# Performance work log

Measured on AMD Instinct MI355X. Metric: run time of the kernel, lower is better.

The kernel has to match this reference:

```python
import jax, jax.numpy as jnp
import numpy as np

B, N = 8, 65536
REG_WEIGHT = 1.0


def box2corners(box):
    # box: (B,N,5) [x,y,w,h,alpha] -> corners (B,N,4,2), CCW order
    x, y, w, h, alpha = (box[..., i] for i in range(5))
    x4 = jnp.asarray([0.5, -0.5, -0.5, 0.5], box.dtype) * w[..., None]
    y4 = jnp.asarray([0.5, 0.5, -0.5, -0.5], box.dtype) * h[..., None]
    c = jnp.cos(alpha)[..., None]
    s = jnp.sin(alpha)[..., None]
    cx = x4 * c - y4 * s + x[..., None]
    cy = x4 * s + y4 * c + y[..., None]
    return jnp.stack([cx, cy], axis=-1)


def box_intersection(c1, c2):
    # all 4x4 edge-pair intersections -> pts (B,N,16,2), mask (B,N,16)
    p1, q1 = c1, jnp.roll(c1, -1, axis=2)
    p2, q2 = c2, jnp.roll(c2, -1, axis=2)
    x1, y1 = p1[..., :, None, 0], p1[..., :, None, 1]
    x2, y2 = q1[..., :, None, 0], q1[..., :, None, 1]
    x3, y3 = p2[..., None, :, 0], p2[..., None, :, 1]
    x4, y4 = q2[..., None, :, 0], q2[..., None, :, 1]
    den = (x4 - x3) * (y1 - y2) - (x1 - x2) * (y4 - y3)
    num_t = (y4 - y3) * (x1 - x3) - (x4 - x3) * (y1 - y3)
    num_u = (y1 - y2) * (x1 - x3) - (x1 - x2) * (y1 - y3)
    safe = jnp.where(den == 0, 1.0, den)
    t = jnp.where(den == 0, -1.0, num_t / safe)
    u = jnp.where(den == 0, -1.0, -num_u / safe)
    mask = (t > 0) & (t < 1) & (u > 0) & (u < 1)
    pts = jnp.stack([x1 + t * (x2 - x1), y1 + t * (y2 - y1)], axis=-1)
    pts = pts * mask[..., None]
    Bb, Nn = c1.shape[0], c1.shape[1]
    return pts.reshape(Bb, Nn, 16, 2), mask.reshape(Bb, Nn, 16)


def box1_in_box2(c1, c2):
    # corners of box1 (B,N,4,2) inside box2 via projection on its edges
    a, b, d = c2[..., 0:1, :], c2[..., 1:2, :], c2[..., 3:4, :]
    ab, ad, ap = b - a, d - a, c1 - a
    pab = jnp.sum(ap * ab, -1) / jnp.sum(ab * ab, -1)
    pad_ = jnp.sum(ap * ad, -1) / jnp.sum(ad * ad, -1)
    eps = 1e-6
    return (pab > -eps) & (pab < 1 + eps) & (pad_ > -eps) & (pad_ < 1 + eps)


def oriented_box_intersection_2d(c1, c2):
    pts, m_i = box_intersection(c1, c2)
    m1 = box1_in_box2(c1, c2)
    m2 = box1_in_box2(c2, c1)
    verts = jnp.concatenate([c1, c2, pts], axis=2)   # (B,N,24,2)
    mask = jnp.concatenate([m1, m2, m_i], axis=2)    # (B,N,24)
    mf = mask[..., None].astype(verts.dtype)
    nv = jnp.maximum(jnp.sum(mf, axis=2, keepdims=True), 1.0)
    mean = jnp.sum(verts * mf, axis=2, keepdims=True) / nv  # (B,N,1,2)
    dxy = verts - mean
    ang = jnp.where(mask, jnp.arctan2(dxy[..., 1], dxy[..., 0]), 1e9)
    order = jnp.argsort(ang, axis=-1)
    sv = jnp.take_along_axis(verts, order[..., None], axis=2)
    sm = jnp.take_along_axis(mask, order, axis=-1)
    # pad invalid slots with the first (smallest-angle) valid vertex -> zero shoelace contribution
    poly = jnp.where(sm[..., None], sv, sv[..., 0:1, :])
    x, y = poly[..., 0], poly[..., 1]
    area = 0.5 * jnp.abs(jnp.sum(x * jnp.roll(y, -1, axis=-1) - jnp.roll(x, -1, axis=-1) * y, axis=-1))
    return area, poly


def diff_iou_rotated_3d(box3d1, box3d2, mode='iou'):
    idx = jnp.asarray([0, 1, 3, 4, 6])
    c1 = box2corners(box3d1[..., idx])
    c2 = box2corners(box3d2[..., idx])
    inter_2d, _ = oriented_box_intersection_2d(c1, c2)
    zmax1 = box3d1[..., 2] + 0.5 * box3d1[..., 5]
    zmin1 = box3d1[..., 2] - 0.5 * box3d1[..., 5]
    zmax2 = box3d2[..., 2] + 0.5 * box3d2[..., 5]
    zmin2 = box3d2[..., 2] - 0.5 * box3d2[..., 5]
    z_overlap = jnp.clip(jnp.minimum(zmax1, zmax2) - jnp.maximum(zmin1, zmin2), 0.0)
    inter_3d = inter_2d * z_overlap
    vol1 = box3d1[..., 3] * box3d1[..., 4] * box3d1[..., 5]
    vol2 = box3d2[..., 3] * box3d2[..., 4] * box3d2[..., 5]
    union = vol1 + vol2 - inter_3d
    iou = inter_3d / union
    if mode == 'iou':
        return iou
    inter_diag = jnp.sum((box3d1[..., 0:3] - box3d2[..., 0:3]) ** 2, axis=-1)
    outer_h = jnp.clip(jnp.maximum(zmax1, zmax2) - jnp.minimum(zmin1, zmin2), 0.0)
    out_max = jnp.maximum(c1[:, :, 2], c2[:, :, 2])
    out_min = jnp.minimum(c1[:, :, 0], c2[:, :, 0])
    outer = jnp.clip(out_max - out_min, 0.0)
    outer_diag = outer[..., 0] ** 2 + outer[..., 1] ** 2 + outer_h ** 2
    return jnp.clip(iou - inter_diag / outer_diag, -1.0, 1.0)


def setup_inputs() -> dict:
    key = jax.random.key(0)
    ks = jax.random.split(key, 5)
    ctr = jax.random.uniform(ks[0], (B, N, 3), minval=-50.0, maxval=50.0)
    dims = jax.random.uniform(ks[1], (B, N, 3), minval=1.0, maxval=5.0)
    ang = jax.random.uniform(ks[2], (B, N, 1), minval=-np.pi, maxval=np.pi)
    pred_boxes = jnp.concatenate([ctr, dims, ang], axis=-1)  # (B,N,7)
    noise = jax.random.normal(ks[3], (B, N, 7)) * jnp.asarray([0.5, 0.5, 0.3, 0.3, 0.3, 0.3, 0.2])
    gt7 = pred_boxes + noise
    gt_dims = jnp.maximum(gt7[..., 3:6], 0.1)
    gt_boxes = jnp.concatenate([gt7[..., :3], gt_dims, jnp.sin(gt7[..., 6:7]), jnp.cos(gt7[..., 6:7])], axis=-1)  # (B,N,8)
    pred_iou = jax.random.uniform(ks[4], (B, N)) * 2.0 - 1.0
    mask = jnp.ones((B, N), dtype=bool)
    return {'pred_iou': pred_iou, 'pred_boxes': pred_boxes, 'gt_boxes': gt_boxes, 'mask': mask}


def reference(pred_iou, pred_boxes, gt_boxes, mask):
    mf = mask.astype(pred_iou.dtype).reshape(-1)
    cnt = jnp.maximum(jnp.sum(mf), 1e-4)
    Bb, Nn = pred_iou.shape
    pb = pred_boxes.reshape(1, Bb * Nn, 7)
    gb = gt_boxes.reshape(1, Bb * Nn, 8)
    ang = jnp.arctan2(gb[..., 6:7], gb[..., 7:8])
    gb7 = jnp.concatenate([gb[..., :6], ang], axis=-1)
    target = diff_iou_rotated_3d(pb, gb7, 'iou').reshape(-1) * 2.0 - 1.0
    iou_loss = jnp.sum(jnp.abs(pred_iou.reshape(-1) - target) * mf) / cnt
    diou = diff_iou_rotated_3d(pb, gb7, 'diou').reshape(-1)
    reg_loss = jnp.sum((1.0 - diou) * mf) / cnt
    return iou_loss + reg_loss * REG_WEIGHT
```

## Files before the change

### kernel.cpp

```cpp
#include <hip/hip_runtime.h>


#define RCPF(x) __builtin_amdgcn_rcpf(x)

struct EIn {
    float b[7];
    float g[8];
    float pred;
    float mf;
};

__device__ __forceinline__ void load_elem(EIn& e,
    const float* __restrict__ pred_iou, const float* __restrict__ pred_boxes,
    const float* __restrict__ gt_boxes, const int* __restrict__ mask, int gid)
{
    const float* pb = pred_boxes + (size_t)gid * 7;
    #pragma unroll
    for (int k = 0; k < 7; ++k) e.b[k] = pb[k];
    const float* gb = gt_boxes + (size_t)gid * 8;
    #pragma unroll
    for (int k = 0; k < 8; ++k) e.g[k] = gb[k];
    e.pred = pred_iou[gid];
    e.mf = (mask[gid] != 0) ? 1.0f : 0.0f;
}

__device__ __forceinline__ float elem_body(const EIn& e)
{
    const float b1x = e.b[0], b1y = e.b[1], b1z = e.b[2];
    const float b1w = e.b[3], b1h = e.b[4], b1l = e.b[5], a1 = e.b[6];
    const float b2x = e.g[0], b2y = e.g[1], b2z = e.g[2];
    const float b2w = e.g[3], b2h = e.g[4], b2l = e.g[5];
    const float gsn = e.g[6], gcs = e.g[7];

    float sn1, cs1;
    __sincosf(a1, &sn1, &cs1);
    const float rn = __builtin_amdgcn_rsqf(gsn * gsn + gcs * gcs);
    const float sn2 = gsn * rn, cs2 = gcs * rn;

    const float xs[4] = {0.5f, -0.5f, -0.5f, 0.5f};
    const float ys[4] = {0.5f, 0.5f, -0.5f, -0.5f};
    float c1x[4], c1y[4], c2x[4], c2y[4];
    #pragma unroll
    for (int k = 0; k < 4; ++k) {
        float xx = xs[k] * b1w, yy = ys[k] * b1h;
        c1x[k] = xx * cs1 - yy * sn1 + b1x;
        c1y[k] = xx * sn1 + yy * cs1 + b1y;
        float x2 = xs[k] * b2w, y2 = ys[k] * b2h;
        c2x[k] = x2 * cs2 - y2 * sn2 + b2x;
        c2y[k] = x2 * sn2 + y2 * cs2 + b2y;
    }

    float vx[24], vy[24];
    unsigned vmask = 0u;
    const float eps = 1e-6f;

    {
        float ax = c2x[0], ay = c2y[0];
        float abx = c2x[1] - ax, aby = c2y[1] - ay;
        float adx = c2x[3] - ax, ady = c2y[3] - ay;
        float ab2 = abx * abx + aby * aby;
        float ad2 = adx * adx + ady * ady;
        float lo_ab = -eps * ab2, hi_ab = (1.0f + eps) * ab2;
        float lo_ad = -eps * ad2, hi_ad = (1.0f + eps) * ad2;
        #pragma unroll
        for (int k = 0; k < 4; ++k) {
            vx[k] = c1x[k]; vy[k] = c1y[k];
            float apx = c1x[k] - ax, apy = c1y[k] - ay;
            float dab = apx * abx + apy * aby;
            float dad = apx * adx + apy * ady;
            bool in2 = (dab > lo_ab) && (dab < hi_ab) && (dad > lo_ad) && (dad < hi_ad);
            vmask |= (in2 ? 1u : 0u) << k;
        }
    }
    {
        float ax = c1x[0], ay = c1y[0];
        float abx = c1x[1] - ax, aby = c1y[1] - ay;
        float adx = c1x[3] - ax, ady = c1y[3] - ay;
        float ab2 = abx * abx + aby * aby;
        float ad2 = adx * adx + ady * ady;
        float lo_ab = -eps * ab2, hi_ab = (1.0f + eps) * ab2;
        float lo_ad = -eps * ad2, hi_ad = (1.0f + eps) * ad2;
        #pragma unroll
        for (int k = 0; k < 4; ++k) {
            vx[4 + k] = c2x[k]; vy[4 + k] = c2y[k];
            float apx = c2x[k] - ax, apy = c2y[k] - ay;
            float dab = apx * abx + apy * aby;
            float dad = apx * adx + apy * ady;
            bool in1 = (dab > lo_ab) && (dab < hi_ab) && (dad > lo_ad) && (dad < hi_ad);
            vmask |= (in1 ? 1u : 0u) << (4 + k);
        }
    }

    float e1dx[4], e1dy[4], e2dx[4], e2dy[4];
    #pragma unroll
    for (int l = 0; l < 4; ++l) {
        e1dx[l] = c1x[l] - c1x[(l + 1) & 3];
        e1dy[l] = c1y[l] - c1y[(l + 1) & 3];
        e2dx[l] = c2x[l] - c2x[(l + 1) & 3];
        e2dy[l] = c2y[l] - c2y[(l + 1) & 3];
    }
    #pragma unroll
    for (int l = 0; l < 4; ++l) {
        float x1 = c1x[l], y1 = c1y[l];
        #pragma unroll
        for (int m = 0; m < 4; ++m) {
            float rx = x1 - c2x[m], ry = y1 - c2y[m];
            float den  = e1dx[l] * e2dy[m] - e2dx[m] * e1dy[l];
            float numt = e2dx[m] * ry - e2dy[m] * rx;
            float numu = e1dx[l] * ry - e1dy[l] * rx;
            float rden = RCPF(den);
            float t = numt * rden;
            float u = numu * rden;
            bool ok = (t > 0.0f) && (t < 1.0f) && (u > 0.0f) && (u < 1.0f);
            int v = 8 + l * 4 + m;
            vx[v] = x1 - t * e1dx[l];
            vy[v] = y1 - t * e1dy[l];
            vmask |= (ok ? 1u : 0u) << v;
        }
    }

    float px[8], py[8];
    #pragma unroll
    for (int j = 0; j < 8; ++j) { px[j] = 0.0f; py[j] = 0.0f; }
    unsigned r = 0u;
    #pragma unroll
    for (int v = 0; v < 24; ++v) {
        #pragma unroll
        for (int j = 0; j < 8; ++j) {
            if (j <= v) {
                bool take = (r == (unsigned)j);
                px[j] = take ? vx[v] : px[j];
                py[j] = take ? vy[v] : py[j];
            }
        }
        r += (vmask >> v) & 1u;
    }
    int kcnt = (int)r;
    if (kcnt > 8) kcnt = 8;

    float sxm = 0.0f, sym = 0.0f;
    #pragma unroll
    for (int j = 0; j < 8; ++j) {
        bool a = (j < kcnt);
        sxm += a ? px[j] : 0.0f;
        sym += a ? py[j] : 0.0f;
    }
    float rnv = RCPF(fmaxf((float)kcnt, 1.0f));
    float mx = sxm * rnv, my = sym * rnv;

    float key[8];
    #pragma unroll
    for (int j = 0; j < 8; ++j) {
        float dx = px[j] - mx, dy = py[j] - my;
        float ad = fabsf(dx) + fabsf(dy);
        float rr = dx * RCPF(fmaxf(ad, 1e-30f));
        float k = __builtin_copysignf(1.0f - rr, dy);
        key[j] = (j < kcnt) ? k : 1e9f;
    }

    #pragma unroll
    for (int kk = 2; kk <= 8; kk <<= 1) {
        #pragma unroll
        for (int j = kk >> 1; j > 0; j >>= 1) {
            #pragma unroll
            for (int t0 = 0; t0 < 8; ++t0) {
                int o = t0 ^ j;
                if (o > t0) {
                    bool up = (t0 & kk) == 0;
                    float ka = key[t0], kb = key[o];
                    bool sw = up ? (ka > kb) : (ka < kb);
                    float xa = px[t0], xb = px[o];
                    float ya = py[t0], yb = py[o];
                    key[t0] = sw ? kb : ka; key[o] = sw ? ka : kb;
                    px[t0]  = sw ? xb : xa; px[o]  = sw ? xa : xb;
                    py[t0]  = sw ? yb : ya; py[o]  = sw ? ya : yb;
                }
            }
        }
    }

    float x0 = px[0], y0 = py[0];
    float area2 = 0.0f;
    #pragma unroll
    for (int v = 0; v < 8; ++v) {
        bool active = (v < kcnt);
        bool wrap = (v + 1 == kcnt);
        float nx2 = (v == 7) ? x0 : (wrap ? x0 : px[v + 1]);
        float ny2 = (v == 7) ? y0 : (wrap ? y0 : py[v + 1]);
        float term = px[v] * ny2 - nx2 * py[v];
        area2 += active ? term : 0.0f;
    }
    float inter2d = 0.5f * fabsf(area2);

    float zmax1 = b1z + 0.5f * b1l, zmin1 = b1z - 0.5f * b1l;
    float zmax2 = b2z + 0.5f * b2l, zmin2 = b2z - 0.5f * b2l;
    float zov = fmaxf(fminf(zmax1, zmax2) - fmaxf(zmin1, zmin2), 0.0f);
    float inter3d = inter2d * zov;
    float vol1 = b1w * b1h * b1l;
    float vol2 = b2w * b2h * b2l;
    float uni = vol1 + vol2 - inter3d;
    float iou = inter3d * RCPF(uni);
    float target = iou * 2.0f - 1.0f;

    float ddx = b1x - b2x, ddy = b1y - b2y, ddz = b1z - b2z;
    float interdiag = ddx * ddx + ddy * ddy + ddz * ddz;
    float outerh = fmaxf(fmaxf(zmax1, zmax2) - fminf(zmin1, zmin2), 0.0f);
    float omx = fmaxf(fmaxf(c1x[2], c2x[2]) - fminf(c1x[0], c2x[0]), 0.0f);
    float omy = fmaxf(fmaxf(c1y[2], c2y[2]) - fminf(c1y[0], c2y[0]), 0.0f);
    float outerdiag = omx * omx + omy * omy + outerh * outerh;
    float diou = iou - interdiag * RCPF(outerdiag);
    diou = fminf(fmaxf(diou, -1.0f), 1.0f);

    return (fabsf(e.pred - target) + (1.0f - diou)) * e.mf;
}

__global__ __launch_bounds__(256, 4) void iou3d_loss_kernel(
    const float* __restrict__ pred_iou,
    const float* __restrict__ pred_boxes,
    const float* __restrict__ gt_boxes,
    const int*   __restrict__ mask,
    float* __restrict__ sums,
    int M)
{
    const int idx0 = blockIdx.x * blockDim.x + threadIdx.x;
    const int stride = gridDim.x * blockDim.x;
    const int idx1 = idx0 + stride;

    float contrib = 0.0f, mfv = 0.0f;

    if (idx1 < M) {
        EIn e0, e1;
        load_elem(e0, pred_iou, pred_boxes, gt_boxes, mask, idx0);
        load_elem(e1, pred_iou, pred_boxes, gt_boxes, mask, idx1);
        contrib = elem_body(e0) + elem_body(e1);
        mfv = e0.mf + e1.mf;
    } else if (idx0 < M) {
        EIn e0;
        load_elem(e0, pred_iou, pred_boxes, gt_boxes, mask, idx0);
        contrib = elem_body(e0);
        mfv = e0.mf;
    }

    #pragma unroll
    for (int off = 32; off > 0; off >>= 1) {
        contrib += __shfl_down(contrib, off, 64);
        mfv     += __shfl_down(mfv, off, 64);
    }
    __shared__ float sC[4], sM[4];
    const int lane = threadIdx.x & 63;
    const int wv = threadIdx.x >> 6;
    if (lane == 0) { sC[wv] = contrib; sM[wv] = mfv; }
    __syncthreads();
    if (threadIdx.x == 0) {
        float tc = sC[0] + sC[1] + sC[2] + sC[3];
        float tm = sM[0] + sM[1] + sM[2] + sM[3];
        atomicAdd(&sums[0], tc);
        atomicAdd(&sums[1], tm);
    }
}

__global__ void finalize_kernel(const float* __restrict__ sums, float* __restrict__ out) {
    if (threadIdx.x == 0 && blockIdx.x == 0)
        out[0] = sums[0] / fmaxf(sums[1], 1e-4f);
}

extern "C" void kernel_launch(void* const* d_in, const int* in_sizes, int n_in,
                              void* d_out, int out_size, void* d_ws, size_t ws_size,
                              hipStream_t stream) {
    const float* pred_iou   = (const float*)d_in[0];
    const float* pred_boxes = (const float*)d_in[1];
    const float* gt_boxes   = (const float*)d_in[2];
    const int*   mask       = (const int*)d_in[3];
    float* out  = (float*)d_out;
    float* sums = (float*)d_ws;
    const int M = in_sizes[0];

    hipMemsetAsync(sums, 0, 2 * sizeof(float), stream);
    const int block = 256;
    const int elems_per_thread = 2;
    int grid = (M + block * elems_per_thread - 1) / (block * elems_per_thread);
    if (grid < 1) grid = 1;
    hipLaunchKernelGGL(iou3d_loss_kernel, dim3(grid), dim3(block), 0, stream,
                       pred_iou, pred_boxes, gt_boxes, mask, sums, M);
    hipLaunchKernelGGL(finalize_kernel, dim3(1), dim3(64), 0, stream, sums, out);
}
```

Measured before the change: 113.1 us.

## Compact valid polygon vertices via per-thread LDS scatter instead of select network

```diff
diff --git a/kernel.cpp b/kernel.cpp
--- a/kernel.cpp
+++ b/kernel.cpp
@@ -12,7 +12,8 @@
 
 __device__ __forceinline__ void load_elem(EIn& e,
     const float* __restrict__ pred_iou, const float* __restrict__ pred_boxes,
-    const float* __restrict__ gt_boxes, const int* __restrict__ mask, int gid)
+    const float* __restrict__ gt_boxes, const int* __restrict__ mask,
+    int gid, bool active)
 {
     const float* pb = pred_boxes + (size_t)gid * 7;
     #pragma unroll
@@ -21,10 +22,10 @@
     #pragma unroll
     for (int k = 0; k < 8; ++k) e.g[k] = gb[k];
     e.pred = pred_iou[gid];
-    e.mf = (mask[gid] != 0) ? 1.0f : 0.0f;
-}
-
-__device__ __forceinline__ float elem_body(const EIn& e)
+    e.mf = (active && mask[gid] != 0) ? 1.0f : 0.0f;
+}
+
+__device__ __forceinline__ float elem_body(const EIn& e, float* __restrict__ sl)
 {
     const float b1x = e.b[0], b1y = e.b[1], b1z = e.b[2];
     const float b1w = e.b[3], b1h = e.b[4], b1l = e.b[5], a1 = e.b[6];
@@ -50,8 +51,9 @@
         c2y[k] = x2 * sn2 + y2 * cs2 + b2y;
     }
 
-    float vx[24], vy[24];
-    unsigned vmask = 0u;
+    float2* slot = reinterpret_cast<float2*>(sl);
+    unsigned r = 0u;
+
     const float eps = 1e-6f;
 
     {
@@ -64,12 +66,13 @@
         float lo_ad = -eps * ad2, hi_ad = (1.0f + eps) * ad2;
         #pragma unroll
         for (int k = 0; k < 4; ++k) {
-            vx[k] = c1x[k]; vy[k] = c1y[k];
             float apx = c1x[k] - ax, apy = c1y[k] - ay;
             float dab = apx * abx + apy * aby;
             float dad = apx * adx + apy * ady;
-            bool in2 = (dab > lo_ab) && (dab < hi_ab) && (dad > lo_ad) && (dad < hi_ad);
-            vmask |= (in2 ? 1u : 0u) << k;
+            bool ok = (dab > lo_ab) && (dab < hi_ab) && (dad > lo_ad) && (dad < hi_ad);
+            unsigned rm = r < 8u ? r : 8u;
+            slot[rm] = make_float2(c1x[k], c1y[k]);
+            r += ok ? 1u : 0u;
         }
     }
     {
@@ -82,12 +85,13 @@
         float lo_ad = -eps * ad2, hi_ad = (1.0f + eps) * ad2;
         #pragma unroll
         for (int k = 0; k < 4; ++k) {
-            vx[4 + k] = c2x[k]; vy[4 + k] = c2y[k];
             float apx = c2x[k] - ax, apy = c2y[k] - ay;
             float dab = apx * abx + apy * aby;
             float dad = apx * adx + apy * ady;
-            bool in1 = (dab > lo_ab) && (dab < hi_ab) && (dad > lo_ad) && (dad < hi_ad);
-            vmask |= (in1 ? 1u : 0u) << (4 + k);
+            bool ok = (dab > lo_ab) && (dab < hi_ab) && (dad > lo_ad) && (dad < hi_ad);
+            unsigned rm = r < 8u ? r : 8u;
+            slot[rm] = make_float2(c2x[k], c2y[k]);
+            r += ok ? 1u : 0u;
         }
     }
 
@@ -108,35 +112,25 @@
             float den  = e1dx[l] * e2dy[m] - e2dx[m] * e1dy[l];
             float numt = e2dx[m] * ry - e2dy[m] * rx;
             float numu = e1dx[l] * ry - e1dy[l] * rx;
-            float rden = RCPF(den);
-            float t = numt * rden;
-            float u = numu * rden;
-            bool ok = (t > 0.0f) && (t < 1.0f) && (u > 0.0f) && (u < 1.0f);
-            int v = 8 + l * 4 + m;
-            vx[v] = x1 - t * e1dx[l];
-            vy[v] = y1 - t * e1dy[l];
-            vmask |= (ok ? 1u : 0u) << v;
+            float aden = fabsf(den);
+            bool ok = (numt * den > 0.0f) && (fabsf(numt) < aden) &&
+                      (numu * den > 0.0f) && (fabsf(numu) < aden);
+            float t = numt * RCPF(den);
+            float X = x1 - t * e1dx[l];
+            float Y = y1 - t * e1dy[l];
+            unsigned rm = r < 8u ? r : 8u;
+            slot[rm] = make_float2(X, Y);
+            r += ok ? 1u : 0u;
         }
     }
 
     float px[8], py[8];
     #pragma unroll
-    for (int j = 0; j < 8; ++j) { px[j] = 0.0f; py[j] = 0.0f; }
-    unsigned r = 0u;
-    #pragma unroll
-    for (int v = 0; v < 24; ++v) {
-        #pragma unroll
-        for (int j = 0; j < 8; ++j) {
-            if (j <= v) {
-                bool take = (r == (unsigned)j);
-                px[j] = take ? vx[v] : px[j];
-                py[j] = take ? vy[v] : py[j];
-            }
-        }
-        r += (vmask >> v) & 1u;
-    }
-    int kcnt = (int)r;
-    if (kcnt > 8) kcnt = 8;
+    for (int j = 0; j < 8; ++j) {
+        float2 p = slot[j];
+        px[j] = p.x; py[j] = p.y;
+    }
+    int kcnt = (int)(r < 8u ? r : 8u);
 
     float sxm = 0.0f, sym = 0.0f;
     #pragma unroll
@@ -222,24 +216,22 @@
     float* __restrict__ sums,
     int M)
 {
+    __shared__ float lds[256 * 38];
+    float* sl0 = &lds[threadIdx.x * 38u];
+    float* sl1 = sl0 + 18;
+
     const int idx0 = blockIdx.x * blockDim.x + threadIdx.x;
     const int stride = gridDim.x * blockDim.x;
     const int idx1 = idx0 + stride;
-
-    float contrib = 0.0f, mfv = 0.0f;
-
-    if (idx1 < M) {
-        EIn e0, e1;
-        load_elem(e0, pred_iou, pred_boxes, gt_boxes, mask, idx0);
-        load_elem(e1, pred_iou, pred_boxes, gt_boxes, mask, idx1);
-        contrib = elem_body(e0) + elem_body(e1);
-        mfv = e0.mf + e1.mf;
-    } else if (idx0 < M) {
-        EIn e0;
-        load_elem(e0, pred_iou, pred_boxes, gt_boxes, mask, idx0);
-        contrib = elem_body(e0);
-        mfv = e0.mf;
-    }
+    const int mlast = M - 1;
+    const int i0 = idx0 < M ? idx0 : mlast;
+    const int i1 = idx1 < M ? idx1 : mlast;
+
+    EIn e0, e1;
+    load_elem(e0, pred_iou, pred_boxes, gt_boxes, mask, i0, idx0 < M);
+    load_elem(e1, pred_iou, pred_boxes, gt_boxes, mask, i1, idx1 < M);
+    float contrib = elem_body(e0, sl0) + elem_body(e1, sl1);
+    float mfv = e0.mf + e1.mf;
 
     #pragma unroll
     for (int off = 32; off > 0; off >>= 1) {
```

After: 112.1 us. No clear change (-0.8%).
